# Performance work log

Hardware: AMD Instinct MI355X
Metric: run time of the kernel (lower is better)

The kernel has to match this reference:

```python
import jax, jax.numpy as jnp
import numpy as np

N_BINS = 15


def setup_inputs() -> dict:
    key = jax.random.key(0)
    k1, k2 = jax.random.split(key)
    N, C = 500000, 100
    logits = jax.random.normal(k1, (N, C), dtype=jnp.float32)
    labels = jax.random.randint(k2, (N,), 0, C, dtype=jnp.int64)
    return {"logits": logits, "labels": labels}


def _classwise_ece(logits, labels, n_bins=N_BINS):
    # Fused equivalent of the per-class, per-bin double loop.
    # Bins are (lower, upper] with boundaries linspace(0,1,n_bins+1),
    # so bin index = ceil(p * n_bins) - 1; p == 0 falls in NO bin.
    probs = jax.nn.softmax(logits, axis=1)            # [N, C]
    N, C = probs.shape
    valid = probs > 0.0                               # p==0 matched by no (lower, upper] bin
    bin_idx = jnp.clip(jnp.ceil(probs * n_bins).astype(jnp.int32) - 1, 0, n_bins - 1)

    class_ids = jnp.arange(C, dtype=jnp.int32)[None, :]          # [1, C]
    key = (jnp.broadcast_to(class_ids * n_bins, probs.shape) + bin_idx).reshape(-1)  # [N*C]

    w = valid.astype(probs.dtype)
    correct = (labels[:, None] == class_ids).astype(probs.dtype)  # labels_in_class

    num_seg = C * n_bins
    count = jax.ops.segment_sum(w.reshape(-1), key, num_segments=num_seg).reshape(C, n_bins)
    conf_sum = jax.ops.segment_sum((probs * w).reshape(-1), key, num_segments=num_seg).reshape(C, n_bins)
    acc_sum = jax.ops.segment_sum((correct * w).reshape(-1), key, num_segments=num_seg).reshape(C, n_bins)

    # |avg_conf - acc| * prop_in_bin == |conf_sum - acc_sum| / N; empty bins give 0.
    per_class_sce = jnp.sum(jnp.abs(conf_sum - acc_sum), axis=1) / N   # [C]
    sce = jnp.mean(per_class_sce)
    return sce, per_class_sce


def reference(logits, labels):
    return _classwise_ece(logits, labels)
```

## Files before the change

### kernel.cpp

```cpp
#include <hip/hip_runtime.h>
#include <math.h>

#define NCLS 100
#define NBINS 15
#define NSEG (NCLS * NBINS)
#define RPI 8

__device__ __forceinline__ void fadd(float* p, float v) { unsafeAtomicAdd(p, v); }

template <int CTRL>
__device__ __forceinline__ float dpp_add(float x) {
    int y = __builtin_amdgcn_update_dpp(0, __builtin_bit_cast(int, x),
                                        CTRL, 0xf, 0xf, true);
    return x + __builtin_bit_cast(float, y);
}

__global__ __launch_bounds__(256) void ece_main_kernel(
    const float* __restrict__ logits,
    const int* __restrict__ labels,
    float* __restrict__ g_total,
    float* __restrict__ g_conf,
    float* __restrict__ g_acc,
    int N)
{
    __shared__ float s_total[NCLS];
    __shared__ float s_conf[NSEG];
    __shared__ float s_acc[NSEG];
    for (int i = threadIdx.x; i < NSEG; i += 256) { s_conf[i] = 0.f; s_acc[i] = 0.f; }
    if (threadIdx.x < NCLS) s_total[threadIdx.x] = 0.f;
    __syncthreads();

    const int lane   = threadIdx.x & 63;
    const int wave   = threadIdx.x >> 6;
    const int gwave  = blockIdx.x * 4 + wave;
    const int nwaves = gridDim.x * 4;

    const int c0 = lane;
    const int c1 = lane + 64;
    const bool has1 = (c1 < NCLS);

    float t0 = 0.f, t1 = 0.f;

    for (int base = gwave * RPI; base < N; base += nwaves * RPI) {
        const int labv = labels[min(base + lane, N - 1)];

        float e0[RPI], e1[RPI], s[RPI];

        #pragma unroll
        for (int r = 0; r < RPI; ++r) {
            const int row = base + r;
            const bool v = (row < N);
            const float* rp = logits + (size_t)row * NCLS;
            e0[r] = v ? rp[c0] : -1000.f;
            e1[r] = (v && has1) ? rp[c1] : -1000.f;
        }

        #pragma unroll
        for (int r = 0; r < RPI; ++r) {
            e0[r] = __expf(e0[r]);
            e1[r] = __expf(e1[r]);
            s[r] = e0[r] + e1[r];
        }

        #pragma unroll
        for (int r = 0; r < RPI; ++r) s[r] = dpp_add<0x111>(s[r]);
        #pragma unroll
        for (int r = 0; r < RPI; ++r) s[r] = dpp_add<0x112>(s[r]);
        #pragma unroll
        for (int r = 0; r < RPI; ++r) s[r] = dpp_add<0x114>(s[r]);
        #pragma unroll
        for (int r = 0; r < RPI; ++r) s[r] = dpp_add<0x118>(s[r]);
        #pragma unroll
        for (int r = 0; r < RPI; ++r) s[r] = dpp_add<0x142>(s[r]);
        #pragma unroll
        for (int r = 0; r < RPI; ++r) s[r] = dpp_add<0x143>(s[r]);

        #pragma unroll
        for (int r = 0; r < RPI; ++r) {
            const float tot = __builtin_bit_cast(float,
                __builtin_amdgcn_readlane(__builtin_bit_cast(int, s[r]), 63));
            const float inv = __builtin_amdgcn_rcpf(fmaxf(tot, 1e-30f));
            const int lab = (base + r < N)
                          ? __builtin_amdgcn_readlane(labv, r) : -1;

            const float p0 = e0[r] * inv;
            t0 += p0;
            int b0 = min((int)ceilf(p0 * 15.f) - 1, NBINS - 1);
            if (b0 >= 1) fadd(&s_conf[c0 * NBINS + b0], p0);
            if (c0 == lab) fadd(&s_acc[c0 * NBINS + max(b0, 0)], 1.f);

            const float p1 = e1[r] * inv;
            t1 += p1;
            int b1 = min((int)ceilf(p1 * 15.f) - 1, NBINS - 1);
            if (b1 >= 1) fadd(&s_conf[c1 * NBINS + b1], p1);
            if (has1 && c1 == lab) fadd(&s_acc[c1 * NBINS + max(b1, 0)], 1.f);
        }
    }

    fadd(&s_total[c0], t0);
    if (has1) fadd(&s_total[c1], t1);
    __syncthreads();

    for (int i = threadIdx.x; i < NSEG; i += 256) {
        float v = s_conf[i]; if (v != 0.f) fadd(&g_conf[i], v);
        float a = s_acc[i];  if (a != 0.f) fadd(&g_acc[i], a);
    }
    if (threadIdx.x < NCLS) {
        float t = s_total[threadIdx.x];
        if (t != 0.f) fadd(&g_total[threadIdx.x], t);
    }
}

__global__ __launch_bounds__(128) void ece_final_kernel(
    const float* __restrict__ g_total,
    const float* __restrict__ g_conf,
    const float* __restrict__ g_acc,
    float* __restrict__ out,
    float invN)
{
    __shared__ float red[128];
    const int t = threadIdx.x;
    float s = 0.f;
    if (t < NCLS) {
        float conf0 = g_total[t];
        float sum = 0.f;
        #pragma unroll
        for (int b = 1; b < NBINS; ++b) {
            float cb = g_conf[t * NBINS + b];
            float ab = g_acc[t * NBINS + b];
            conf0 -= cb;
            sum += fabsf(cb - ab);
        }
        sum += fabsf(conf0 - g_acc[t * NBINS + 0]);
        s = sum * invN;
        out[1 + t] = s;
    }
    red[t] = s;
    __syncthreads();
    #pragma unroll
    for (int off = 64; off > 0; off >>= 1) {
        if (t < off) red[t] += red[t + off];
        __syncthreads();
    }
    if (t == 0) out[0] = red[0] * (1.0f / (float)NCLS);
}

extern "C" void kernel_launch(void* const* d_in, const int* in_sizes, int n_in,
                              void* d_out, int out_size, void* d_ws, size_t ws_size,
                              hipStream_t stream)
{
    const float* logits = (const float*)d_in[0];
    const int*   labels = (const int*)d_in[1];
    const int N = in_sizes[1];
    float* out = (float*)d_out;

    float* g_total = (float*)d_ws;
    float* g_conf  = g_total + NCLS;
    float* g_acc   = g_conf + NSEG;

    (void)hipMemsetAsync(d_ws, 0, (size_t)(NCLS + 2 * NSEG) * sizeof(float), stream);

    const int blocks = 2048;
    ece_main_kernel<<<blocks, 256, 0, stream>>>(logits, labels,
                                                g_total, g_conf, g_acc, N);
    ece_final_kernel<<<1, 128, 0, stream>>>(g_total, g_conf, g_acc, out,
                                            1.0f / (float)N);
}
```

Baseline: 351.3 us.

## Double-buffer tile loads, use float2 loads, and reduce partial histograms in a separate kernel

The main loop now prefetches the next 8-row tile into a second register buffer while the current tile is processed, with a sched barrier so the loads are issued first. Each lane now loads two adjacent classes with a single float2 load instead of two strided scalar loads. The grid is halved to 1024 blocks with occupancy hints. Per-block histograms are written as non-temporal partials to workspace and summed by a new reduce kernel, replacing global float atomics. This costs more registers, an extra kernel launch and extra workspace traffic.

```diff
diff --git a/kernel.cpp b/kernel.cpp
--- a/kernel.cpp
+++ b/kernel.cpp
@@ -4,9 +4,16 @@
 #define NCLS 100
 #define NBINS 15
 #define NSEG (NCLS * NBINS)
+#define NTOT (2 * NSEG + NCLS)
+#define PSTRIDE 3104
 #define RPI 8
+#define GMAIN 1024
 
 __device__ __forceinline__ void fadd(float* p, float v) { unsafeAtomicAdd(p, v); }
+
+__device__ __forceinline__ float readlane_f(float x, int l) {
+    return __builtin_bit_cast(float, __builtin_amdgcn_readlane(__builtin_bit_cast(int, x), l));
+}
 
 template <int CTRL>
 __device__ __forceinline__ float dpp_add(float x) {
@@ -15,17 +22,86 @@
     return x + __builtin_bit_cast(float, y);
 }
 
-__global__ __launch_bounds__(256) void ece_main_kernel(
+__device__ __forceinline__ void load_tile(
+    const float* __restrict__ logits, const int* __restrict__ labels,
+    int base, int N, int lane, bool act,
+    float (&e0)[RPI], float (&e1)[RPI], int& labv)
+{
+    labv = labels[min(base + lane, N - 1)];
+    const float* rp = logits + (size_t)base * NCLS + 2 * lane;
+    if (base + RPI <= N) {
+        #pragma unroll
+        for (int r = 0; r < RPI; ++r) {
+            float2 v = make_float2(-1000.f, -1000.f);
+            if (act) v = *(const float2*)(rp + (size_t)r * NCLS);
+            e0[r] = v.x; e1[r] = v.y;
+        }
+    } else {
+        #pragma unroll
+        for (int r = 0; r < RPI; ++r) {
+            float2 v = make_float2(-1000.f, -1000.f);
+            if (act && (base + r) < N) v = *(const float2*)(rp + (size_t)r * NCLS);
+            e0[r] = v.x; e1[r] = v.y;
+        }
+    }
+}
+
+__device__ __forceinline__ void compute_tile(
+    int base, int N, int lane, bool act, int c0, int c1,
+    float (&e0)[RPI], float (&e1)[RPI], int labv,
+    float& t0, float& t1, float* s_conf, float* s_acc)
+{
+    float s[RPI];
+    #pragma unroll
+    for (int r = 0; r < RPI; ++r) {
+        e0[r] = __expf(e0[r]);
+        e1[r] = __expf(e1[r]);
+        s[r] = e0[r] + e1[r];
+    }
+    #pragma unroll
+    for (int r = 0; r < RPI; ++r) s[r] = dpp_add<0x111>(s[r]);
+    #pragma unroll
+    for (int r = 0; r < RPI; ++r) s[r] = dpp_add<0x112>(s[r]);
+    #pragma unroll
+    for (int r = 0; r < RPI; ++r) s[r] = dpp_add<0x114>(s[r]);
+    #pragma unroll
+    for (int r = 0; r < RPI; ++r) s[r] = dpp_add<0x118>(s[r]);
+    #pragma unroll
+    for (int r = 0; r < RPI; ++r) s[r] = dpp_add<0x142>(s[r]);
+    #pragma unroll
+    for (int r = 0; r < RPI; ++r) s[r] = dpp_add<0x143>(s[r]);
+
+    #pragma unroll
+    for (int r = 0; r < RPI; ++r) {
+        const float tot = readlane_f(s[r], 63);
+        const float inv = __builtin_amdgcn_rcpf(fmaxf(tot, 1e-30f));
+        const int lab = (base + r < N)
+                      ? __builtin_amdgcn_readlane(labv, r) : -1;
+        const float p0 = e0[r] * inv;
+        const float p1 = e1[r] * inv;
+        t0 += p0;
+        t1 += p1;
+        if (act) {
+            int b0 = min((int)ceilf(p0 * 15.f) - 1, NBINS - 1);
+            if (b0 >= 1) fadd(&s_conf[c0 * NBINS + b0], p0);
+            if (c0 == lab) fadd(&s_acc[c0 * NBINS + max(b0, 0)], 1.f);
+            int b1 = min((int)ceilf(p1 * 15.f) - 1, NBINS - 1);
+            if (b1 >= 1) fadd(&s_conf[c1 * NBINS + b1], p1);
+            if (c1 == lab) fadd(&s_acc[c1 * NBINS + max(b1, 0)], 1.f);
+        }
+    }
+}
+
+__global__ __launch_bounds__(256, 4) void ece_main_kernel(
     const float* __restrict__ logits,
     const int* __restrict__ labels,
-    float* __restrict__ g_total,
-    float* __restrict__ g_conf,
-    float* __restrict__ g_acc,
+    float* __restrict__ g_hist,
+    float* __restrict__ parts,
     int N)
 {
-    __shared__ float s_total[NCLS];
     __shared__ float s_conf[NSEG];
     __shared__ float s_acc[NSEG];
+    __shared__ float s_total[NCLS];
     for (int i = threadIdx.x; i < NSEG; i += 256) { s_conf[i] = 0.f; s_acc[i] = 0.f; }
     if (threadIdx.x < NCLS) s_total[threadIdx.x] = 0.f;
     __syncthreads();
@@ -34,87 +110,87 @@
     const int wave   = threadIdx.x >> 6;
     const int gwave  = blockIdx.x * 4 + wave;
     const int nwaves = gridDim.x * 4;
-
-    const int c0 = lane;
-    const int c1 = lane + 64;
-    const bool has1 = (c1 < NCLS);
+    const bool act   = (lane < NCLS / 2);
+    const int c0 = 2 * lane;
+    const int c1 = 2 * lane + 1;
 
     float t0 = 0.f, t1 = 0.f;
 
-    for (int base = gwave * RPI; base < N; base += nwaves * RPI) {
-        const int labv = labels[min(base + lane, N - 1)];
-
-        float e0[RPI], e1[RPI], s[RPI];
-
-        #pragma unroll
-        for (int r = 0; r < RPI; ++r) {
-            const int row = base + r;
-            const bool v = (row < N);
-            const float* rp = logits + (size_t)row * NCLS;
-            e0[r] = v ? rp[c0] : -1000.f;
-            e1[r] = (v && has1) ? rp[c1] : -1000.f;
-        }
-
-        #pragma unroll
-        for (int r = 0; r < RPI; ++r) {
-            e0[r] = __expf(e0[r]);
-            e1[r] = __expf(e1[r]);
-            s[r] = e0[r] + e1[r];
-        }
-
-        #pragma unroll
-        for (int r = 0; r < RPI; ++r) s[r] = dpp_add<0x111>(s[r]);
-        #pragma unroll
-        for (int r = 0; r < RPI; ++r) s[r] = dpp_add<0x112>(s[r]);
-        #pragma unroll
-        for (int r = 0; r < RPI; ++r) s[r] = dpp_add<0x114>(s[r]);
-        #pragma unroll
-        for (int r = 0; r < RPI; ++r) s[r] = dpp_add<0x118>(s[r]);
-        #pragma unroll
-        for (int r = 0; r < RPI; ++r) s[r] = dpp_add<0x142>(s[r]);
-        #pragma unroll
-        for (int r = 0; r < RPI; ++r) s[r] = dpp_add<0x143>(s[r]);
-
-        #pragma unroll
-        for (int r = 0; r < RPI; ++r) {
-            const float tot = __builtin_bit_cast(float,
-                __builtin_amdgcn_readlane(__builtin_bit_cast(int, s[r]), 63));
-            const float inv = __builtin_amdgcn_rcpf(fmaxf(tot, 1e-30f));
-            const int lab = (base + r < N)
-                          ? __builtin_amdgcn_readlane(labv, r) : -1;
-
-            const float p0 = e0[r] * inv;
-            t0 += p0;
-            int b0 = min((int)ceilf(p0 * 15.f) - 1, NBINS - 1);
-            if (b0 >= 1) fadd(&s_conf[c0 * NBINS + b0], p0);
-            if (c0 == lab) fadd(&s_acc[c0 * NBINS + max(b0, 0)], 1.f);
-
-            const float p1 = e1[r] * inv;
-            t1 += p1;
-            int b1 = min((int)ceilf(p1 * 15.f) - 1, NBINS - 1);
-            if (b1 >= 1) fadd(&s_conf[c1 * NBINS + b1], p1);
-            if (has1 && c1 == lab) fadd(&s_acc[c1 * NBINS + max(b1, 0)], 1.f);
-        }
-    }
-
-    fadd(&s_total[c0], t0);
-    if (has1) fadd(&s_total[c1], t1);
-    __syncthreads();
-
-    for (int i = threadIdx.x; i < NSEG; i += 256) {
-        float v = s_conf[i]; if (v != 0.f) fadd(&g_conf[i], v);
-        float a = s_acc[i];  if (a != 0.f) fadd(&g_acc[i], a);
-    }
-    if (threadIdx.x < NCLS) {
-        float t = s_total[threadIdx.x];
-        if (t != 0.f) fadd(&g_total[threadIdx.x], t);
+    float A0[RPI], A1[RPI], B0[RPI], B1[RPI];
+    int labA = 0, labB = 0;
+    const int step = nwaves * RPI;
+    int base = gwave * RPI;
+    bool curA = true;
+    if (base < N) load_tile(logits, labels, base, N, lane, act, A0, A1, labA);
+    while (base < N) {
+        const int nxt = base + step;
+        if (curA) {
+            if (nxt < N) {
+                load_tile(logits, labels, nxt, N, lane, act, B0, B1, labB);
+                __builtin_amdgcn_sched_barrier(0);
+            }
+            compute_tile(base, N, lane, act, c0, c1, A0, A1, labA, t0, t1, s_conf, s_acc);
+        } else {
+            if (nxt < N) {
+                load_tile(logits, labels, nxt, N, lane, act, A0, A1, labA);
+                __builtin_amdgcn_sched_barrier(0);
+            }
+            compute_tile(base, N, lane, act, c0, c1, B0, B1, labB, t0, t1, s_conf, s_acc);
+        }
+        curA = !curA;
+        base = nxt;
+    }
+
+    if (act) { fadd(&s_total[c0], t0); fadd(&s_total[c1], t1); }
+    __syncthreads();
+
+    if (parts) {
+        float* my = parts + (size_t)blockIdx.x * PSTRIDE;
+        for (int i = threadIdx.x; i < NSEG; i += 256) {
+            __builtin_nontemporal_store(s_conf[i], &my[i]);
+            __builtin_nontemporal_store(s_acc[i], &my[NSEG + i]);
+        }
+        if (threadIdx.x < NCLS)
+            __builtin_nontemporal_store(s_total[threadIdx.x], &my[2 * NSEG + threadIdx.x]);
+    } else {
+        for (int i = threadIdx.x; i < NSEG; i += 256) {
+            float v = s_conf[i]; if (v != 0.f) fadd(&g_hist[i], v);
+            float a = s_acc[i];  if (a != 0.f) fadd(&g_hist[NSEG + i], a);
+        }
+        if (threadIdx.x < NCLS) {
+            float t = s_total[threadIdx.x];
+            if (t != 0.f) fadd(&g_hist[2 * NSEG + threadIdx.x], t);
+        }
+    }
+}
+
+__global__ __launch_bounds__(256) void ece_reduce_kernel(
+    const float* __restrict__ parts, float* __restrict__ g_hist, int nparts)
+{
+    const int lane = threadIdx.x & 63;
+    const int wave = threadIdx.x >> 6;
+    const int cell = blockIdx.x * 64 + lane;
+    const int nchunks = gridDim.y * 4;
+    const int chunk = blockIdx.y * 4 + wave;
+    const int per = nparts / nchunks;
+    float s = 0.f;
+    if (cell < NTOT) {
+        const float* bp = parts + (size_t)chunk * per * PSTRIDE + cell;
+        #pragma unroll 8
+        for (int p = 0; p < per; ++p)
+            s += __builtin_nontemporal_load(&bp[(size_t)p * PSTRIDE]);
+    }
+    __shared__ float red[4][64];
+    red[wave][lane] = s;
+    __syncthreads();
+    if (wave == 0) {
+        float v = red[0][lane] + red[1][lane] + red[2][lane] + red[3][lane];
+        if (cell < NTOT && v != 0.f) fadd(&g_hist[cell], v);
     }
 }
 
 __global__ __launch_bounds__(128) void ece_final_kernel(
-    const float* __restrict__ g_total,
-    const float* __restrict__ g_conf,
-    const float* __restrict__ g_acc,
+    const float* __restrict__ g_hist,
     float* __restrict__ out,
     float invN)
 {
@@ -122,16 +198,16 @@
     const int t = threadIdx.x;
     float s = 0.f;
     if (t < NCLS) {
-        float conf0 = g_total[t];
+        float conf0 = g_hist[2 * NSEG + t];
         float sum = 0.f;
         #pragma unroll
         for (int b = 1; b < NBINS; ++b) {
-            float cb = g_conf[t * NBINS + b];
-            float ab = g_acc[t * NBINS + b];
+            float cb = g_hist[t * NBINS + b];
+            float ab = g_hist[NSEG + t * NBINS + b];
             conf0 -= cb;
             sum += fabsf(cb - ab);
         }
-        sum += fabsf(conf0 - g_acc[t * NBINS + 0]);
+        sum += fabsf(conf0 - g_hist[NSEG + t * NBINS + 0]);
         s = sum * invN;
         out[1 + t] = s;
     }
@@ -154,15 +230,17 @@
     const int N = in_sizes[1];
     float* out = (float*)d_out;
 
-    float* g_total = (float*)d_ws;
-    float* g_conf  = g_total + NCLS;
-    float* g_acc   = g_conf + NSEG;
-
-    (void)hipMemsetAsync(d_ws, 0, (size_t)(NCLS + 2 * NSEG) * sizeof(float), stream);
-
-    const int blocks = 2048;
-    ece_main_kernel<<<blocks, 256, 0, stream>>>(logits, labels,
-                                                g_total, g_conf, g_acc, N);
-    ece_final_kernel<<<1, 128, 0, stream>>>(g_total, g_conf, g_acc, out,
-                                            1.0f / (float)N);
-}
+    float* g_hist = (float*)d_ws;
+    const size_t parts_off = ((size_t)NTOT * sizeof(float) + 255) & ~(size_t)255;
+    const size_t need = parts_off + (size_t)GMAIN * PSTRIDE * sizeof(float);
+    float* parts = (ws_size >= need) ? (float*)((char*)d_ws + parts_off) : nullptr;
+
+    (void)hipMemsetAsync(d_ws, 0, (size_t)NTOT * sizeof(float), stream);
+
+    ece_main_kernel<<<GMAIN, 256, 0, stream>>>(logits, labels, g_hist, parts, N);
+    if (parts) {
+        dim3 g2((NTOT + 63) / 64, 4);
+        ece_reduce_kernel<<<g2, 256, 0, stream>>>(parts, g_hist, GMAIN);
+    }
+    ece_final_kernel<<<1, 128, 0, stream>>>(g_hist, out, 1.0f / (float)N);
+}
```

Result: faster. 299.9 us (-14.6%).
